# Optimization experiments

Measured on AMD Instinct MI355X. Metric: run time of the kernel, lower is better.

Reference implementation:

```python
import jax, jax.numpy as jnp
import numpy as np

NUM_HEADS = 16
D_MODEL = 1024
HEAD_DIM = D_MODEL // NUM_HEADS
EMB = 1024
B, L = 2, 2048


def setup_inputs() -> dict:
    key = jax.random.key(0)
    k1, k2, k3 = jax.random.split(key, 3)
    scale_in = 1.0 / np.sqrt(EMB)
    scale_out = 1.0 / np.sqrt(D_MODEL)
    return {
        "x": jax.random.normal(k1, (B, L, EMB), dtype=jnp.float32),
        "W_qkv": jax.random.normal(k2, (EMB, 3 * D_MODEL), dtype=jnp.float32) * scale_in,
        "b_qkv": jnp.zeros((3 * D_MODEL,), dtype=jnp.float32),
        "W_out": jax.random.normal(k3, (D_MODEL, EMB), dtype=jnp.float32) * scale_out,
        "b_out": jnp.zeros((EMB,), dtype=jnp.float32),
    }


def reference(x, W_qkv, b_qkv, W_out, b_out):
    Bn, Ln, _ = x.shape
    qkv = x @ W_qkv + b_qkv  # [B, L, 3*d_model]
    q = qkv[:, :, :D_MODEL].reshape(Bn, Ln, NUM_HEADS, HEAD_DIM)
    k = qkv[:, :, D_MODEL:2 * D_MODEL].reshape(Bn, Ln, NUM_HEADS, HEAD_DIM)
    v = qkv[:, :, 2 * D_MODEL:].reshape(Bn, Ln, NUM_HEADS, HEAD_DIM)
    scores = jnp.einsum('bqhd,bkhd->bhqk', q, k)  # [B, H, L, L]
    attn = jax.nn.softmax(scores / jnp.sqrt(jnp.float32(HEAD_DIM)), axis=-1)
    out = jnp.einsum('bhqk,bkhd->bqhd', attn, v).reshape(Bn, Ln, D_MODEL)
    return out @ W_out + b_out
```

## Files before the change

### kernel.cpp

```cpp
#include <hip/hip_runtime.h>
#include <stdint.h>

#define B_   2
#define L_   2048
#define H_   16
#define D_   64
#define EMB_ 1024
#define DM_  1024
#define N3_  3072
#define TOK_ 4096

typedef unsigned short u16;
typedef unsigned int u32;
typedef __attribute__((ext_vector_type(4))) float f32x4;
typedef __attribute__((ext_vector_type(8))) short s16x8;
typedef __attribute__((ext_vector_type(4))) short s16x4;
typedef __attribute__((ext_vector_type(4))) u32 u32x4;
typedef __attribute__((ext_vector_type(2))) u32 u32x2;
typedef __attribute__((ext_vector_type(4))) u16 u16x4;

#define MFMA(a,b,c) __builtin_amdgcn_mfma_f32_16x16x32_bf16(a,b,c,0,0,0)

#if defined(__has_builtin)
#if __has_builtin(__builtin_amdgcn_mfma_f32_16x16x16bf16_1k)
#define MFMA16(a,b,c) __builtin_amdgcn_mfma_f32_16x16x16bf16_1k(a,b,c,0,0,0)
#endif
#endif
#ifndef MFMA16
static __device__ __forceinline__ f32x4 mfma16_asm(s16x4 a, s16x4 b, f32x4 c) {
  asm volatile("v_mfma_f32_16x16x16_bf16 %0, %1, %2, %0"
               : "+v"(c) : "v"(a), "v"(b));
  return c;
}
#define MFMA16(a,b,c) mfma16_asm(a,b,c)
#endif

#define AS1 __attribute__((address_space(1)))
#define AS3 __attribute__((address_space(3)))
#define GLLDS(g, l) __builtin_amdgcn_global_load_lds( \
    (const AS1 u32*)(const void*)(g), (AS3 u32*)(void*)(l), 16, 0, 0)

#define QSCALE 0.18033688011f

static __device__ __forceinline__ u16 f2bf(float f) {
  u32 u = __builtin_bit_cast(u32, f);
  return (u16)((u + 0x8000u) >> 16);
}

static __device__ __forceinline__ float bf2f(u16 v) {
  u32 u = ((u32)v) << 16;
  return __builtin_bit_cast(float, u);
}

static __device__ __forceinline__ u16 f2h(float f) {
  _Float16 h = (_Float16)f;
  return __builtin_bit_cast(u16, h);
}

static __device__ __forceinline__ float h2f(u16 v) {
  _Float16 h = __builtin_bit_cast(_Float16, v);
  return (float)h;
}

static __device__ __forceinline__ u32 pack2bf(float a, float b) {
  u32 ua = __builtin_bit_cast(u32, a) + 0x8000u;
  u32 ub = __builtin_bit_cast(u32, b) + 0x8000u;
  return __builtin_amdgcn_perm(ub, ua, 0x07060302u);
}

static __device__ __forceinline__ float fexp2(float x) {
#if __has_builtin(__builtin_amdgcn_exp2f)
  return __builtin_amdgcn_exp2f(x);
#else
  float r;
  asm("v_exp_f32 %0, %1" : "=v"(r) : "v"(x));
  return r;
#endif
}

__global__ __launch_bounds__(256) void k_prep(
    const float* __restrict__ x,   u16* __restrict__ xb,
    const float* __restrict__ Wq,  u16* __restrict__ wqT,
    const float* __restrict__ Wo,  u16* __restrict__ woT)
{
  const int blk = blockIdx.x, tid = threadIdx.x;
  if (blk < 4096) {
    int i = (blk * 256 + tid) * 4;
    float4 v = *(const float4*)(x + i);
    ushort4 o;
    o.x = f2bf(v.x); o.y = f2bf(v.y); o.z = f2bf(v.z); o.w = f2bf(v.w);
    *(ushort4*)(xb + i) = o;
    return;
  }
  __shared__ float tile[32][33];
  const float* in;
  u16* out;
  int R, C, bx, by;
  if (blk < 4096 + 3072) {
    int t = blk - 4096;
    in = Wq; out = wqT; R = EMB_; C = N3_;
    bx = t % 96; by = t / 96;
  } else {
    int t = blk - 7168;
    in = Wo; out = woT; R = DM_; C = DM_;
    bx = t & 31; by = t >> 5;
  }
  int c0 = bx * 32, r0 = by * 32;
  int tx = tid & 31, ty = tid >> 5;
  #pragma unroll
  for (int i = 0; i < 32; i += 8)
    tile[ty + i][tx] = in[(size_t)(r0 + ty + i) * C + (c0 + tx)];
  __syncthreads();
  int c = tid >> 3, j = tid & 7;
  u16x4 o;
  #pragma unroll
  for (int r = 0; r < 4; ++r)
    o[r] = f2bf(tile[j * 4 + r][c]);
  *(u16x4*)(out + (size_t)(c0 + c) * R + r0 + j * 4) = o;
}

template<int EPI, int BN>
__global__ __launch_bounds__(256, 4) void k_gemm(
    const u16* __restrict__ A, const u16* __restrict__ Bt,
    const float* __restrict__ bias, int M, int N, int K,
    float* __restrict__ Cf,
    u16* __restrict__ Qo, u16* __restrict__ Ko, u16* __restrict__ Vo)
{
  constexpr int NF = BN / 32;
  constexpr int BROWS = (BN == 128) ? 32 : 16;
  const int tid = threadIdx.x;
  const int wave = tid >> 6, lane = tid & 63;
  const int lr = lane & 15, lk = lane >> 4;
  const int wr = wave >> 1, wc = wave & 1;
  const int m0 = blockIdx.y * 128, n0 = blockIdx.x * BN;

  __shared__ u16 As[2][128 * 32];
  __shared__ u16 Bs[2][BN * 32];

  f32x4 acc[4][NF] = {};

  const int srow = wave * 32 + (lane >> 2);
  const int srowB = (BN == 128) ? srow : (wave * 16 + (lane >> 2));
  const int schunk = (lane & 3) * 8;
  const u16* gA = A  + (size_t)(m0 + srow) * K + schunk;
  const u16* gB = Bt + (size_t)(n0 + srowB) * K + schunk;
  const size_t rstep = (size_t)16 * K;
  u16* lA0 = (u16*)As[0] + wave * (32 * 32);
  u16* lA1 = (u16*)As[1] + wave * (32 * 32);
  u16* lB0 = (u16*)Bs[0] + wave * (BROWS * 32);
  u16* lB1 = (u16*)Bs[1] + wave * (BROWS * 32);

  GLLDS(gA,         lA0);
  GLLDS(gA + rstep, lA0 + 16 * 32);
  GLLDS(gB,         lB0);
  if (BN == 128) GLLDS(gB + rstep, lB0 + 16 * 32);

  int buf = 0;
  for (int k0 = 0; k0 < K; k0 += 32, buf ^= 1) {
    __syncthreads();

    if (k0 + 32 < K) {
      u16* dA = buf ? lA0 : lA1;
      u16* dB = buf ? lB0 : lB1;
      GLLDS(gA + k0 + 32,         dA);
      GLLDS(gA + k0 + 32 + rstep, dA + 16 * 32);
      GLLDS(gB + k0 + 32,         dB);
      if (BN == 128) GLLDS(gB + k0 + 32 + rstep, dB + 16 * 32);
    }

    const u16* Ab = (const u16*)As[buf];
    const u16* Bb = (const u16*)Bs[buf];
    s16x8 af[4], bfr[NF];
    #pragma unroll
    for (int mi = 0; mi < 4; ++mi)
      af[mi] = *(const s16x8*)(Ab + (wr * 64 + mi * 16 + lr) * 32 + lk * 8);
    #pragma unroll
    for (int ni = 0; ni < NF; ++ni)
      bfr[ni] = *(const s16x8*)(Bb + (wc * (BN / 2) + ni * 16 + lr) * 32 + lk * 8);
    #pragma unroll
    for (int mi = 0; mi < 4; ++mi)
      #pragma unroll
      for (int ni = 0; ni < NF; ++ni)
        acc[mi][ni] = MFMA(af[mi], bfr[ni], acc[mi][ni]);
  }

  const int mbase = m0 + wr * 64 + lk * 4;
  #pragma unroll
  for (int ni = 0; ni < NF; ++ni) {
    int gn = n0 + wc * (BN / 2) + ni * 16 + lr;
    float bz = bias[gn];
    if (EPI == 1) {
      #pragma unroll
      for (int mi = 0; mi < 4; ++mi)
        #pragma unroll
        for (int r = 0; r < 4; ++r) {
          int gm = mbase + mi * 16 + r;
          Cf[(size_t)gm * N + gn] = acc[mi][ni][r] + bz;
        }
    } else {
      int sec = gn >> 10, cm = gn & 1023;
      int h = cm >> 6, d = cm & 63;
      if (sec == 2) {
        #pragma unroll
        for (int mi = 0; mi < 4; ++mi) {
          int gm0 = mbase + mi * 16;
          int b = gm0 >> 11, l0 = gm0 & 2047;
          int bh = b * H_ + h;
          u16x4 vv;
          #pragma unroll
          for (int r = 0; r < 4; ++r) vv[r] = f2bf(acc[mi][ni][r] + bz);
          *(u16x4*)(Vo + ((size_t)bh * D_ + d) * L_ + l0) = vv;
        }
      } else {
        #pragma unroll
        for (int mi = 0; mi < 4; ++mi)
          #pragma unroll
          for (int r = 0; r < 4; ++r) {
            int gm = mbase + mi * 16 + r;
            float v = acc[mi][ni][r] + bz;
            int b = gm >> 11, l = gm & 2047;
            int bh = b * H_ + h;
            if (sec == 0) Qo[((size_t)bh * L_ + l) * D_ + d] = f2bf(v * QSCALE);
            else          Ko[((size_t)bh * L_ + l) * D_ + d] = f2bf(v);
          }
      }
    }
  }
}

#define KSTAGE(kb_, vb_, tn_) do { \
    u16* kd_ = (u16*)(kb_) + wave * (16 * 64); \
    u16* vd_ = (u16*)(vb_) + wave * (16 * 64); \
    GLLDS(Kh + (size_t)((tn_) + srow0) * 64 + gch8,       kd_); \
    GLLDS(Kh + (size_t)((tn_) + srow0 + 8) * 64 + gch8,   kd_ + 8 * 64); \
    GLLDS(Vh + ((size_t)srow0 * L_ + (tn_) + gch8),       vd_); \
    GLLDS(Vh + ((size_t)(srow0 + 8) * L_ + (tn_) + gch8), vd_ + 8 * 64); \
  } while (0)

__global__ __launch_bounds__(256, 2) void k_flash(
    const u16* __restrict__ Q, const u16* __restrict__ Kb,
    const u16* __restrict__ Vt,
    u16* __restrict__ O0, u16* __restrict__ O1, float* __restrict__ lpart)
{
  const int tid = threadIdx.x;
  const int wave = tid >> 6, lane = tid & 63;
  const int lr = lane & 15, lk = lane >> 4;
  const int blk = blockIdx.x;
  const int idx = blk >> 3;
  const int bh = (blk & 7) * 4 + (idx >> 4);
  const int rem = idx & 15;
  const int qt = rem >> 1;
  const int half = rem & 1;
  const int tbase = half * 1024;
  const int b = bh >> 4, h = bh & 15;
  const u16* Qh = Q  + (size_t)bh * L_ * D_;
  const u16* Kh = Kb + (size_t)bh * L_ * D_;
  const u16* Vh = Vt + (size_t)bh * D_ * L_;

  __shared__ u16 Ks[3][64 * 64];
  __shared__ u16 Vs[3][64 * 64];

  const int qrow0 = qt * 256 + wave * 64;
  s16x8 qf[4][2];
  #pragma unroll
  for (int g = 0; g < 4; ++g)
    #pragma unroll
    for (int ks = 0; ks < 2; ++ks)
      qf[g][ks] = *(const s16x8*)(Qh + (size_t)(qrow0 + g * 16 + lr) * D_ + ks * 32 + lk * 8);

  f32x4 acco[4][4] = {};
  float lst[4] = {0.f, 0.f, 0.f, 0.f};
  const f32x4 zz = {0.f, 0.f, 0.f, 0.f};

  const int srow0 = wave * 16 + (lane >> 3);
  const int gch8 = (((lane & 7) ^ ((lane >> 3) & 7)) * 8);

  const int sx7 = lr & 7;
  const int ck0 = (lk ^ sx7) * 8;
  const int vsub = (lk & 1) * 4;
  const int vx = lk >> 1;

  KSTAGE(Ks[0], Vs[0], tbase);
  KSTAGE(Ks[1], Vs[1], tbase + 64);

  int c = 0, n = 1, p = 2;
  #pragma unroll 1
  for (int i = 0; i < 16; ++i) {
    if (i < 15) { asm volatile("s_waitcnt vmcnt(4)" ::: "memory"); }
    else        { asm volatile("s_waitcnt vmcnt(0)" ::: "memory"); }
    __builtin_amdgcn_s_barrier();
    asm volatile("" ::: "memory");

    if (i + 2 < 16)
      KSTAGE(Ks[p], Vs[p], tbase + (i + 2) * 64);

    const u16* Kbuf = (const u16*)Ks[c];
    const u16* Vbuf = (const u16*)Vs[c];
    #pragma unroll
    for (int mi = 0; mi < 4; ++mi) {
      const u16* rp = Kbuf + (mi * 16 + lr) * 64;
      s16x8 kf0 = *(const s16x8*)(rp + ck0);
      s16x8 kf1 = *(const s16x8*)(rp + (ck0 ^ 32));
      const int vofs = ((2 * mi + vx) ^ sx7) * 8 + vsub;
      s16x4 vf[4];
      #pragma unroll
      for (int di = 0; di < 4; ++di)
        vf[di] = *(const s16x4*)(Vbuf + (di * 16 + lr) * 64 + vofs);
      #pragma unroll
      for (int g = 0; g < 4; ++g) {
        f32x4 s = MFMA(kf0, qf[g][0], zz);
        s = MFMA(kf1, qf[g][1], s);
        float p0 = fexp2(s[0]), p1 = fexp2(s[1]);
        float p2 = fexp2(s[2]), p3 = fexp2(s[3]);
        lst[g] += (p0 + p1) + (p2 + p3);
        u32x2 pw = { pack2bf(p0, p1), pack2bf(p2, p3) };
        s16x4 pk = __builtin_bit_cast(s16x4, pw);
        #pragma unroll
        for (int di = 0; di < 4; ++di)
          acco[g][di] = MFMA16(vf[di], pk, acco[g][di]);
      }
    }

    int rot = c; c = n; n = p; p = rot;
  }

  u16* Oh = half ? O1 : O0;
  #pragma unroll
  for (int g = 0; g < 4; ++g) {
    float l = lst[g];
    l += __shfl_xor(l, 16);
    l += __shfl_xor(l, 32);
    const int q = qrow0 + g * 16 + lr;
    if (lk == 0)
      lpart[((size_t)(half << 5) + bh) * L_ + q] = l;
    #pragma unroll
    for (int di = 0; di < 4; ++di) {
      u16x4 o;
      #pragma unroll
      for (int r = 0; r < 4; ++r)
        o[r] = f2h(acco[g][di][r]);
      *(u16x4*)(Oh + (size_t)(b * L_ + q) * DM_ + h * D_ + di * 16 + lk * 4) = o;
    }
  }
}

__global__ __launch_bounds__(256) void k_comb(
    const u16* __restrict__ O0, const u16* __restrict__ O1,
    const float* __restrict__ lpart, u16* __restrict__ AO)
{
  const int row = blockIdx.x;
  const int b = row >> 11, l = row & 2047;
  const int c = threadIdx.x * 4;
  const int h = c >> 6;
  const size_t bhl = (size_t)(b * H_ + h) * L_ + l;
  const float rl = 1.0f / (lpart[bhl] + lpart[(size_t)32 * L_ + bhl]);
  const size_t off = (size_t)row * DM_ + c;
  u16x4 a = *(const u16x4*)(O0 + off);
  u16x4 bb = *(const u16x4*)(O1 + off);
  u16x4 o;
  #pragma unroll
  for (int r = 0; r < 4; ++r)
    o[r] = f2bf((h2f(a[r]) + h2f(bb[r])) * rl);
  *(u16x4*)(AO + off) = o;
}

extern "C" void kernel_launch(void* const* d_in, const int* in_sizes, int n_in,
                              void* d_out, int out_size, void* d_ws, size_t ws_size,
                              hipStream_t stream)
{
  const float* x    = (const float*)d_in[0];
  const float* Wqkv = (const float*)d_in[1];
  const float* bqkv = (const float*)d_in[2];
  const float* Wout = (const float*)d_in[3];
  const float* bout = (const float*)d_in[4];
  float* out = (float*)d_out;

  u16* xb  = (u16*)d_ws;
  u16* wqT = xb  + (size_t)TOK_ * EMB_;
  u16* woT = wqT + (size_t)N3_ * EMB_;
  u16* qb  = woT + (size_t)DM_ * EMB_;
  u16* kb  = qb  + (size_t)B_ * H_ * L_ * D_;
  u16* vt  = kb  + (size_t)B_ * H_ * L_ * D_;
  u16* ao  = vt  + (size_t)B_ * H_ * L_ * D_;
  float* lpart = (float*)wqT;

  k_prep<<<4096 + 3072 + 1024, 256, 0, stream>>>(x, xb, Wqkv, wqT, Wout, woT);
  k_gemm<0, 128><<<dim3(N3_ / 128, TOK_ / 128), 256, 0, stream>>>(
      xb, wqT, bqkv, TOK_, N3_, EMB_, nullptr, qb, kb, vt);
  k_flash<<<512, 256, 0, stream>>>(qb, kb, vt, ao, xb, lpart);
  k_comb<<<TOK_, 256, 0, stream>>>(ao, xb, lpart, ao);
  k_gemm<1, 64><<<dim3(DM_ / 64, TOK_ / 128), 256, 0, stream>>>(
      ao, woT, bout, TOK_, DM_, EMB_, out, nullptr, nullptr, nullptr);
}
```

Baseline: 191.9 us.

## Store Q/K/V in MFMA-fragment order and load directly from global, dropping LDS staging

The QKV projection epilogue now writes Q, K and V in a pre-swizzled layout that matches the per-lane MFMA fragment order. The flash kernel then loads K and V fragments straight from global memory with contiguous per-lane vector loads, removing the LDS triple buffer, the barriers and the waitcnt pipelining. Because LDS is no longer used, launch bounds are raised to 4 blocks per CU to increase occupancy. The trade-off is that each wave re-reads K/V from global or L2 without sharing through LDS, and there is no explicit prefetch, so load latency now has to be hidden by occupancy alone.

New measurement: 486.0 us. +153.2%, slower.

```diff
diff --git a/kernel.cpp b/kernel.cpp
--- a/kernel.cpp
+++ b/kernel.cpp
@@ -15,7 +15,6 @@
 typedef __attribute__((ext_vector_type(4))) float f32x4;
 typedef __attribute__((ext_vector_type(8))) short s16x8;
 typedef __attribute__((ext_vector_type(4))) short s16x4;
-typedef __attribute__((ext_vector_type(4))) u32 u32x4;
 typedef __attribute__((ext_vector_type(2))) u32 u32x2;
 typedef __attribute__((ext_vector_type(4))) u16 u16x4;
 
@@ -201,43 +200,42 @@
       int sec = gn >> 10, cm = gn & 1023;
       int h = cm >> 6, d = cm & 63;
       if (sec == 2) {
+        int di = d >> 4, lrf = d & 15;
         #pragma unroll
         for (int mi = 0; mi < 4; ++mi) {
           int gm0 = mbase + mi * 16;
-          int b = gm0 >> 11, l0 = gm0 & 2047;
-          int bh = b * H_ + h;
+          int bb = gm0 >> 11, l0 = gm0 & 2047;
+          int bh = bb * H_ + h;
+          int T = l0 >> 6, mif = (l0 >> 4) & 3, lkf = (l0 >> 2) & 3;
           u16x4 vv;
           #pragma unroll
           for (int r = 0; r < 4; ++r) vv[r] = f2bf(acc[mi][ni][r] + bz);
-          *(u16x4*)(Vo + ((size_t)bh * D_ + d) * L_ + l0) = vv;
+          *(u16x4*)(Vo + (size_t)bh * 131072 +
+                    ((((T * 4 + mif) * 4) + di) << 8) + ((lkf * 16 + lrf) << 2)) = vv;
         }
       } else {
+        int ks = d >> 5, lkq = (d >> 3) & 3, j = d & 7;
+        u16* base = (sec == 0) ? Qo : Ko;
         #pragma unroll
-        for (int mi = 0; mi < 4; ++mi)
+        for (int mi = 0; mi < 4; ++mi) {
+          int gm0 = mbase + mi * 16;
+          int bb = gm0 >> 11, l0 = gm0 & 2047;
+          int bh = bb * H_ + h;
+          int G = l0 >> 4, lrq0 = l0 & 15;
+          u16* dst = base + (size_t)bh * 131072 + ((G * 2 + ks) << 9) + j;
           #pragma unroll
           for (int r = 0; r < 4; ++r) {
-            int gm = mbase + mi * 16 + r;
             float v = acc[mi][ni][r] + bz;
-            int b = gm >> 11, l = gm & 2047;
-            int bh = b * H_ + h;
-            if (sec == 0) Qo[((size_t)bh * L_ + l) * D_ + d] = f2bf(v * QSCALE);
-            else          Ko[((size_t)bh * L_ + l) * D_ + d] = f2bf(v);
+            dst[(lkq * 16 + lrq0 + r) << 3] =
+                (sec == 0) ? f2bf(v * QSCALE) : f2bf(v);
           }
+        }
       }
     }
   }
 }
 
-#define KSTAGE(kb_, vb_, tn_) do { \
-    u16* kd_ = (u16*)(kb_) + wave * (16 * 64); \
-    u16* vd_ = (u16*)(vb_) + wave * (16 * 64); \
-    GLLDS(Kh + (size_t)((tn_) + srow0) * 64 + gch8,       kd_); \
-    GLLDS(Kh + (size_t)((tn_) + srow0 + 8) * 64 + gch8,   kd_ + 8 * 64); \
-    GLLDS(Vh + ((size_t)srow0 * L_ + (tn_) + gch8),       vd_); \
-    GLLDS(Vh + ((size_t)(srow0 + 8) * L_ + (tn_) + gch8), vd_ + 8 * 64); \
-  } while (0)
-
-__global__ __launch_bounds__(256, 2) void k_flash(
+__global__ __launch_bounds__(256, 4) void k_flash(
     const u16* __restrict__ Q, const u16* __restrict__ Kb,
     const u16* __restrict__ Vt,
     u16* __restrict__ O0, u16* __restrict__ O1, float* __restrict__ lpart)
@@ -251,61 +249,38 @@
   const int rem = idx & 15;
   const int qt = rem >> 1;
   const int half = rem & 1;
-  const int tbase = half * 1024;
   const int b = bh >> 4, h = bh & 15;
-  const u16* Qh = Q  + (size_t)bh * L_ * D_;
-  const u16* Kh = Kb + (size_t)bh * L_ * D_;
-  const u16* Vh = Vt + (size_t)bh * D_ * L_;
-
-  __shared__ u16 Ks[3][64 * 64];
-  __shared__ u16 Vs[3][64 * 64];
+
+  const u16* qp = Q  + (size_t)bh * (L_ * D_) + lane * 8;
+  const u16* kp = Kb + (size_t)bh * (L_ * D_) + lane * 8;
+  const u16* vp = Vt + (size_t)bh * (L_ * D_) + lane * 4;
 
   const int qrow0 = qt * 256 + wave * 64;
+  const int G0 = qrow0 >> 4;
   s16x8 qf[4][2];
   #pragma unroll
   for (int g = 0; g < 4; ++g)
     #pragma unroll
     for (int ks = 0; ks < 2; ++ks)
-      qf[g][ks] = *(const s16x8*)(Qh + (size_t)(qrow0 + g * 16 + lr) * D_ + ks * 32 + lk * 8);
+      qf[g][ks] = *(const s16x8*)(qp + (size_t)((G0 + g) * 2 + ks) * 512);
 
   f32x4 acco[4][4] = {};
   float lst[4] = {0.f, 0.f, 0.f, 0.f};
   const f32x4 zz = {0.f, 0.f, 0.f, 0.f};
 
-  const int srow0 = wave * 16 + (lane >> 3);
-  const int gch8 = (((lane & 7) ^ ((lane >> 3) & 7)) * 8);
-
-  const int sx7 = lr & 7;
-  const int ck0 = (lk ^ sx7) * 8;
-  const int vsub = (lk & 1) * 4;
-  const int vx = lk >> 1;
-
-  KSTAGE(Ks[0], Vs[0], tbase);
-  KSTAGE(Ks[1], Vs[1], tbase + 64);
-
-  int c = 0, n = 1, p = 2;
-  #pragma unroll 1
+  const int T0 = half * 16;
   for (int i = 0; i < 16; ++i) {
-    if (i < 15) { asm volatile("s_waitcnt vmcnt(4)" ::: "memory"); }
-    else        { asm volatile("s_waitcnt vmcnt(0)" ::: "memory"); }
-    __builtin_amdgcn_s_barrier();
-    asm volatile("" ::: "memory");
-
-    if (i + 2 < 16)
-      KSTAGE(Ks[p], Vs[p], tbase + (i + 2) * 64);
-
-    const u16* Kbuf = (const u16*)Ks[c];
-    const u16* Vbuf = (const u16*)Vs[c];
+    const int T = T0 + i;
     #pragma unroll
     for (int mi = 0; mi < 4; ++mi) {
-      const u16* rp = Kbuf + (mi * 16 + lr) * 64;
-      s16x8 kf0 = *(const s16x8*)(rp + ck0);
-      s16x8 kf1 = *(const s16x8*)(rp + (ck0 ^ 32));
-      const int vofs = ((2 * mi + vx) ^ sx7) * 8 + vsub;
+      const int kblk = (T * 4 + mi) * 2;
+      s16x8 kf0 = *(const s16x8*)(kp + (size_t)kblk * 512);
+      s16x8 kf1 = *(const s16x8*)(kp + (size_t)(kblk + 1) * 512);
+      const int vblk = (T * 4 + mi) * 4;
       s16x4 vf[4];
       #pragma unroll
       for (int di = 0; di < 4; ++di)
-        vf[di] = *(const s16x4*)(Vbuf + (di * 16 + lr) * 64 + vofs);
+        vf[di] = *(const s16x4*)(vp + (size_t)(vblk + di) * 256);
       #pragma unroll
       for (int g = 0; g < 4; ++g) {
         f32x4 s = MFMA(kf0, qf[g][0], zz);
@@ -320,8 +295,6 @@
           acco[g][di] = MFMA16(vf[di], pk, acco[g][di]);
       }
     }
-
-    int rot = c; c = n; n = p; p = rot;
   }
 
   u16* Oh = half ? O1 : O0;
```
